# Kernel optimization log

Hardware: AMD Instinct MI355X
Metric: run time of the kernel (lower is better)

Reference implementation:

```python
import jax, jax.numpy as jnp
import numpy as np

H = 1024
NH = 16
DH = H // NH
EPS = 1e-12


def _heads(x):
    # [B,T,H] -> [B,NH,T,DH]
    B, T, _ = x.shape
    return x.reshape(B, T, NH, DH).transpose(0, 2, 1, 3)


def _layernorm(x, g, b):
    mu = jnp.mean(x, axis=-1, keepdims=True)
    var = jnp.mean(jnp.square(x - mu), axis=-1, keepdims=True)
    return (x - mu) * jax.lax.rsqrt(var + EPS) * g + b


def setup_inputs() -> dict:
    key = jax.random.key(0)
    ks = jax.random.split(key, 24)
    B, Tw, Te = 4, 1024, 128
    s = 0.02
    inp = {
        "word_hidden_states": jax.random.normal(ks[0], (B, Tw, H), jnp.float32),
        "entity_hidden_states": jax.random.normal(ks[1], (B, Te, H), jnp.float32),
        "attention_mask": jnp.zeros((B, 1, 1, Tw + Te), jnp.float32),
        "query_pos": jax.random.normal(ks[2], (B, Te, H), jnp.float32),
    }
    names = ["Wq", "Wk", "Wv", "Weq", "Wek", "Wev", "Wo", "Weo"]
    for i, n in enumerate(names):
        inp[n] = jax.random.normal(ks[3 + i], (H, H), jnp.float32) * s
        inp["b" + n[1:]] = jnp.zeros((H,), jnp.float32)
    inp["ln_g"] = jnp.ones((H,), jnp.float32)
    inp["ln_b"] = jnp.zeros((H,), jnp.float32)
    inp["eln_g"] = jnp.ones((H,), jnp.float32)
    inp["eln_b"] = jnp.zeros((H,), jnp.float32)
    return inp


def reference(word_hidden_states, entity_hidden_states, attention_mask, query_pos,
              Wq, bq, Wk, bk, Wv, bv, Weq, beq, Wek, bek, Wev, bev,
              Wo, bo, Weo, beo, ln_g, ln_b, eln_g, eln_b):
    Tw = word_hidden_states.shape[1]
    pos_ent = (entity_hidden_states + query_pos) * 0.5

    # per-stream projections (entity stream has its own e2w projections)
    qw = _heads(word_hidden_states @ Wq + bq)      # [B,NH,Tw,DH]
    qe = _heads(pos_ent @ Weq + beq)               # [B,NH,Te,DH]
    kw = _heads(word_hidden_states @ Wk + bk)
    ke = _heads(pos_ent @ Wek + bek)
    vw = _heads(word_hidden_states @ Wv + bv)
    ve = _heads(entity_hidden_states @ Wev + bev)  # value uses raw entity states

    q = jnp.concatenate([qw, qe], axis=2)          # [B,NH,T,DH]
    k = jnp.concatenate([kw, ke], axis=2)
    v = jnp.concatenate([vw, ve], axis=2)

    scores = jnp.einsum("bhqd,bhkd->bhqk", q, k) / np.sqrt(DH).astype(np.float32)
    scores = scores + attention_mask
    probs = jax.nn.softmax(scores, axis=-1)
    ctx = jnp.einsum("bhqk,bhkd->bhqd", probs, v)  # [B,NH,T,DH]
    B, _, T, _ = ctx.shape
    ctx = ctx.transpose(0, 2, 1, 3).reshape(B, T, H)

    word_self = ctx[:, :Tw, :]
    ent_self = ctx[:, Tw:, :]

    word_out = _layernorm(word_self @ Wo + bo + word_hidden_states, ln_g, ln_b)
    ent_out = _layernorm(ent_self @ Weo + beo + entity_hidden_states, eln_g, eln_b)
    return (word_out, ent_out)
```

## Files before the change

### kernel.cpp

```cpp
#include <hip/hip_runtime.h>
#include <math.h>

#define H_DIM 1024
#define NHEAD 16
#define DHEAD 64
#define T_W 1024
#define T_E 128
#define T_T 1152
#define BATCH 4

typedef __attribute__((ext_vector_type(8))) short s8b;
typedef __attribute__((ext_vector_type(4))) short s4b;
typedef __attribute__((ext_vector_type(4))) float f32x4;

#define LOG2E 1.44269504088896f

__device__ __forceinline__ unsigned short f2bf(float f) {
    unsigned int u = __float_as_uint(f);
    u = (u + 0x7fffu + ((u >> 16) & 1u)) >> 16;
    return (unsigned short)u;
}

__device__ __forceinline__ unsigned int pk_bf16(float a, float b) {
#if __has_builtin(__builtin_amdgcn_cvt_pk_bf16_f32)
    typedef __bf16 bf2 __attribute__((ext_vector_type(2)));
    bf2 r = __builtin_amdgcn_cvt_pk_bf16_f32(a, b);
    return __builtin_bit_cast(unsigned int, r);
#else
    return (unsigned int)f2bf(a) | ((unsigned int)f2bf(b) << 16);
#endif
}

__device__ __forceinline__ float exp2f_fast(float x) {
#if __has_builtin(__builtin_amdgcn_exp2f)
    return __builtin_amdgcn_exp2f(x);
#else
    return exp2f(x);
#endif
}

__device__ __forceinline__ void gld_lds16(const void* g, void* l) {
    __builtin_amdgcn_global_load_lds(
        (const __attribute__((address_space(1))) unsigned int*)g,
        (__attribute__((address_space(3))) unsigned int*)l, 16, 0, 0);
}

struct WPtrs { const float* w[8]; };
__global__ __launch_bounds__(256) void k_prep2(
    const float* __restrict__ word, const float* __restrict__ ent,
    const float* __restrict__ qp, const float* __restrict__ mask,
    unsigned short* __restrict__ word_bf, unsigned short* __restrict__ pe_bf,
    unsigned short* __restrict__ ent_bf, float* __restrict__ mask2,
    WPtrs ws, unsigned short* __restrict__ Wt)
{
    const int bid = blockIdx.x;
    if (bid < 4096) {
        int i = bid * 256 + threadIdx.x;
        float4 v = ((const float4*)word)[i];
        *(uint2*)(word_bf + (size_t)i * 4) =
            make_uint2(pk_bf16(v.x, v.y), pk_bf16(v.z, v.w));
    } else if (bid < 4608) {
        int i = (bid - 4096) * 256 + threadIdx.x;
        float4 a = ((const float4*)ent)[i];
        float4 b = ((const float4*)qp)[i];
        *(uint2*)(ent_bf + (size_t)i * 4) =
            make_uint2(pk_bf16(a.x, a.y), pk_bf16(a.z, a.w));
        *(uint2*)(pe_bf + (size_t)i * 4) =
            make_uint2(pk_bf16((a.x + b.x) * 0.5f, (a.y + b.y) * 0.5f),
                       pk_bf16((a.z + b.z) * 0.5f, (a.w + b.w) * 0.5f));
    } else if (bid < 4626) {
        int i = (bid - 4608) * 256 + threadIdx.x;
        if (i < BATCH * T_T) mask2[i] = mask[i] * LOG2E;
    } else {
        __shared__ float tile[32][33];
        const int id = bid - 4626;
        const int z = id >> 10, rem = id & 1023;
        const int kb = (rem >> 5) * 32, nb = (rem & 31) * 32;
        const float* src = ws.w[z];
        unsigned short* dst = Wt + (size_t)z * H_DIM * H_DIM;
        const int tx = threadIdx.x & 31, ty = threadIdx.x >> 5;
        #pragma unroll
        for (int i = 0; i < 4; i++)
            tile[ty * 4 + i][tx] = src[(size_t)(kb + ty * 4 + i) * H_DIM + nb + tx];
        __syncthreads();
        #pragma unroll
        for (int i = 0; i < 4; i++)
            dst[(size_t)(nb + ty * 4 + i) * H_DIM + kb + tx] =
                f2bf(tile[tx][ty * 4 + i]);
    }
}

struct B6 { const float* b[6]; };
struct O3p { void* o[3]; };


__global__ __launch_bounds__(256) void k_proj(
    const unsigned short* __restrict__ word_bf,
    const unsigned short* __restrict__ pe_bf,
    const unsigned short* __restrict__ ent_bf,
    const unsigned short* __restrict__ Wtbase, B6 biases, O3p outs)
{
    const int z = blockIdx.z;
    const bool isw = blockIdx.y < 64;
    const int Tseq = isw ? T_W : T_E;
    const int toff = isw ? 0 : T_W;
    const int m0 = (isw ? blockIdx.y : (blockIdx.y - 64)) * 64;
    const unsigned short* A = isw ? word_bf : (z == 2 ? ent_bf : pe_bf);
    const int wi = (isw ? 0 : 3) + z;
    const unsigned short* B = Wtbase + (size_t)wi * H_DIM * H_DIM;
    const float* bias = biases.b[wi];
    void* outp = outs.o[z];

    __shared__ unsigned short sm[12288];
    const int t = threadIdx.x;
    const int w = t >> 6, lane = t & 63;
    const int col = lane & 15, quad = lane >> 4;
    const int n0 = blockIdx.x * 128;
    const int wm = w & 1, wn = w >> 1;

    f32x4 acc[2][4] = {};

    const int rs = t >> 3;
    const int gch = (t & 7) ^ (rs & 7);
    const unsigned short* gA = A + (size_t)(m0 + rs) * H_DIM + gch * 8;
    const unsigned short* gB = B + (size_t)(n0 + rs) * H_DIM + gch * 8;

    for (int k0 = 0; k0 < H_DIM; k0 += 64) {
        gld_lds16(gA + k0, &sm[t * 8]);
        gld_lds16(gA + (size_t)32 * H_DIM + k0, &sm[2048 + t * 8]);
        gld_lds16(gB + k0, &sm[4096 + t * 8]);
        gld_lds16(gB + (size_t)32 * H_DIM + k0, &sm[6144 + t * 8]);
        gld_lds16(gB + (size_t)64 * H_DIM + k0, &sm[8192 + t * 8]);
        gld_lds16(gB + (size_t)96 * H_DIM + k0, &sm[10240 + t * 8]);
        __syncthreads();
        #pragma unroll
        for (int kk = 0; kk < 2; kk++) {
            s8b af[2], bfr[4];
            #pragma unroll
            for (int mt = 0; mt < 2; mt++) {
                const int r = wm * 32 + mt * 16 + col;
                af[mt] = *(const s8b*)&sm[r * 64 + (((kk * 4 + quad) ^ (r & 7)) * 8)];
            }
            #pragma unroll
            for (int nt = 0; nt < 4; nt++) {
                const int r = wn * 64 + nt * 16 + col;
                bfr[nt] = *(const s8b*)&sm[4096 + r * 64 +
                                           (((kk * 4 + quad) ^ (r & 7)) * 8)];
            }
            __builtin_amdgcn_s_setprio(1);
            #pragma unroll
            for (int mt = 0; mt < 2; mt++)
                #pragma unroll
                for (int nt = 0; nt < 4; nt++)
                    acc[mt][nt] = __builtin_amdgcn_mfma_f32_16x16x32_bf16(
                        af[mt], bfr[nt], acc[mt][nt], 0, 0, 0);
            __builtin_amdgcn_s_setprio(0);
        }
        __syncthreads();
    }

    #pragma unroll
    for (int mt = 0; mt < 2; mt++) {
        const int mg = m0 + wm * 32 + mt * 16 + quad * 4;
        const int b = mg / Tseq, tt = toff + (mg % Tseq);
        #pragma unroll
        for (int nt = 0; nt < 4; nt++) {
            const int ng = n0 + wn * 64 + nt * 16 + col;
            f32x4 c = acc[mt][nt];
            const float bn = bias[ng];
            if (z < 2) {
                unsigned short* out = (unsigned short*)outp;
                #pragma unroll
                for (int r = 0; r < 4; r++)
                    out[((size_t)b * T_T + tt + r) * H_DIM + ng] = f2bf(c[r] + bn);
            } else {
                unsigned short* out = (unsigned short*)outp;
                *(uint2*)(out + ((size_t)b * H_DIM + ng) * T_T + tt) =
                    make_uint2(pk_bf16(c[0] + bn, c[1] + bn),
                               pk_bf16(c[2] + bn, c[3] + bn));
            }
        }
    }
}

__global__ __launch_bounds__(256) void k_gemm_out(
    const unsigned short* __restrict__ ctx,
    const unsigned short* __restrict__ Wt_o, const unsigned short* __restrict__ Wt_eo,
    const float* __restrict__ bo, const float* __restrict__ beo,
    const float* __restrict__ word, const float* __restrict__ ent,
    float* __restrict__ out_word, float* __restrict__ out_ent)
{
    const int blk = blockIdx.x;
    const bool is_word = blk < 512;
    const int lb = is_word ? blk : blk - 512;
    const int m0 = (lb >> 3) * 64, n0 = (lb & 7) * 128;
    const unsigned short* B = is_word ? Wt_o : Wt_eo;
    const float* bias = is_word ? bo : beo;
    const float* resid = is_word ? word : ent;
    float* out = is_word ? out_word : out_ent;
    const int Tseq = is_word ? T_W : T_E;
    const int toff = is_word ? 0 : T_W;

    __shared__ unsigned short sm[12288];
    const int t = threadIdx.x;
    const int w = t >> 6, lane = t & 63;
    const int col = lane & 15, quad = lane >> 4;
    const int wm = w & 1, wn = w >> 1;

    f32x4 acc[2][4] = {};

    const int rs = t >> 3;
    const int gch = (t & 7) ^ (rs & 7);
    const size_t arow = (size_t)(m0 / Tseq) * T_T + toff + (m0 % Tseq) + rs;
    const unsigned short* gA = ctx + arow * H_DIM + gch * 8;
    const unsigned short* gB = B + (size_t)(n0 + rs) * H_DIM + gch * 8;

    for (int k0 = 0; k0 < H_DIM; k0 += 64) {
        gld_lds16(gA + k0, &sm[t * 8]);
        gld_lds16(gA + (size_t)32 * H_DIM + k0, &sm[2048 + t * 8]);
        gld_lds16(gB + k0, &sm[4096 + t * 8]);
        gld_lds16(gB + (size_t)32 * H_DIM + k0, &sm[6144 + t * 8]);
        gld_lds16(gB + (size_t)64 * H_DIM + k0, &sm[8192 + t * 8]);
        gld_lds16(gB + (size_t)96 * H_DIM + k0, &sm[10240 + t * 8]);
        __syncthreads();
        #pragma unroll
        for (int kk = 0; kk < 2; kk++) {
            s8b af[2], bfr[4];
            #pragma unroll
            for (int mt = 0; mt < 2; mt++) {
                const int r = wm * 32 + mt * 16 + col;
                af[mt] = *(const s8b*)&sm[r * 64 + (((kk * 4 + quad) ^ (r & 7)) * 8)];
            }
            #pragma unroll
            for (int nt = 0; nt < 4; nt++) {
                const int r = wn * 64 + nt * 16 + col;
                bfr[nt] = *(const s8b*)&sm[4096 + r * 64 +
                                           (((kk * 4 + quad) ^ (r & 7)) * 8)];
            }
            __builtin_amdgcn_s_setprio(1);
            #pragma unroll
            for (int mt = 0; mt < 2; mt++)
                #pragma unroll
                for (int nt = 0; nt < 4; nt++)
                    acc[mt][nt] = __builtin_amdgcn_mfma_f32_16x16x32_bf16(
                        af[mt], bfr[nt], acc[mt][nt], 0, 0, 0);
            __builtin_amdgcn_s_setprio(0);
        }
        __syncthreads();
    }

    #pragma unroll
    for (int mt = 0; mt < 2; mt++) {
        const int mg = m0 + wm * 32 + mt * 16 + quad * 4;
        #pragma unroll
        for (int nt = 0; nt < 4; nt++) {
            const int ng = n0 + wn * 64 + nt * 16 + col;
            f32x4 c = acc[mt][nt];
            const float bn = bias[ng];
            #pragma unroll
            for (int r = 0; r < 4; r++) {
                const size_t idx = (size_t)(mg + r) * H_DIM + ng;
                out[idx] = c[r] + bn + resid[idx];
            }
        }
    }
}

__global__ __launch_bounds__(512) void k_attn(
    const unsigned short* __restrict__ q, const unsigned short* __restrict__ k,
    const unsigned short* __restrict__ vt, const float* __restrict__ mask2,
    unsigned short* __restrict__ ctx)
{
    const int tid = threadIdx.x;
    const int w = tid >> 6, lane = tid & 63;
    const int col = lane & 15, quad = lane >> 4;
    const int bid = blockIdx.x;
    const int bh = ((bid & 7) << 3) | ((bid >> 3) & 7);
    const int q0 = (bid >> 6) * 128 + w * 16;
    const int b = bh >> 4, h = bh & 15;

    __shared__ unsigned short sK[2][64 * 64];
    __shared__ unsigned short sV[2][64 * 64];
    __shared__ __align__(16) unsigned short sP[8][16 * 64];
    unsigned short* sp = &sP[w][0];

    const unsigned short* qp = q + ((size_t)b * T_T + q0) * H_DIM + h * DHEAD;
    const unsigned short* kp = k + (size_t)b * T_T * H_DIM + h * DHEAD;
    const unsigned short* vp = vt + ((size_t)b * H_DIM + h * DHEAD) * T_T;
    const float* mp = mask2 + (size_t)b * T_T;

    const s8b qf0 = *(const s8b*)(qp + (size_t)col * H_DIM + quad * 8);
    const s8b qf1 = *(const s8b*)(qp + (size_t)col * H_DIM + 32 + quad * 8);

    const int rA = tid >> 3;
    const int cA = (tid & 7) ^ (rA & 7);

    const float SC2 = 0.125f * LOG2E;

    f32x4 O[4] = {};
    float l_part = 0.f;

    #define PREFETCH(J0, BUF)                                                        \
        {                                                                            \
            gld_lds16(kp + (size_t)((J0) + rA) * H_DIM + cA * 8,                     \
                      &sK[BUF][0] + tid * 8);                                        \
            gld_lds16(vp + (size_t)rA * T_T + (J0) + cA * 8,                         \
                      &sV[BUF][0] + tid * 8);                                        \
        }

    PREFETCH(0, 0)
    for (int it = 0; it < 18; it++) {
        const int j0 = it * 64;
        __syncthreads();
        if (it < 17) PREFETCH(j0 + 64, (it + 1) & 1)
        const unsigned short* K0 = &sK[it & 1][0];
        const unsigned short* V0 = &sV[it & 1][0];

        float p[16];
        #pragma unroll
        for (int kt = 0; kt < 4; kt++) {
            const int rk = kt * 16 + col;
            const int csw = quad ^ (rk & 7);
            s8b k0f = *(const s8b*)(K0 + rk * 64 + csw * 8);
            s8b k1f = *(const s8b*)(K0 + rk * 64 + (csw ^ 4) * 8);
            f32x4 z = {0.f, 0.f, 0.f, 0.f};
            __builtin_amdgcn_s_setprio(1);
            z = __builtin_amdgcn_mfma_f32_16x16x32_bf16(k0f, qf0, z, 0, 0, 0);
            z = __builtin_amdgcn_mfma_f32_16x16x32_bf16(k1f, qf1, z, 0, 0, 0);
            __builtin_amdgcn_s_setprio(0);
            float4 mv = *(const float4*)(mp + j0 + kt * 16 + quad * 4);
            float mvv[4] = {mv.x, mv.y, mv.z, mv.w};
            #pragma unroll
            for (int r = 0; r < 4; r++) {
                float pe = exp2f_fast(fmaf(z[r], SC2, mvv[r]));
                p[kt * 4 + r] = pe;
                l_part += pe;
            }
        }

        #pragma unroll
        for (int kt = 0; kt < 4; kt++) {
            const int chunk = 2 * kt + (quad >> 1);
            *(uint2*)(sp + col * 64 + ((chunk ^ (col & 7)) * 8) + (quad & 1) * 4) =
                make_uint2(pk_bf16(p[4 * kt], p[4 * kt + 1]),
                           pk_bf16(p[4 * kt + 2], p[4 * kt + 3]));
        }
        const s8b p0 = *(const s8b*)(sp + col * 64 + ((quad ^ (col & 7)) * 8));
        const s8b p1 = *(const s8b*)(sp + col * 64 + (((4 + quad) ^ (col & 7)) * 8));

        __builtin_amdgcn_s_setprio(1);
        #pragma unroll
        for (int dt = 0; dt < 4; dt++) {
            const int rf = dt * 16 + col;
            const int csw = quad ^ (rf & 7);
            s8b v0 = *(const s8b*)(V0 + rf * 64 + csw * 8);
            s8b v1 = *(const s8b*)(V0 + rf * 64 + (csw ^ 4) * 8);
            O[dt] = __builtin_amdgcn_mfma_f32_16x16x32_bf16(v0, p0, O[dt], 0, 0, 0);
            O[dt] = __builtin_amdgcn_mfma_f32_16x16x32_bf16(v1, p1, O[dt], 0, 0, 0);
        }
        __builtin_amdgcn_s_setprio(0);
    }
    #undef PREFETCH

    float l_c = l_part;
    l_c += __shfl_xor(l_c, 16);
    l_c += __shfl_xor(l_c, 32);
    const float inv = 1.f / l_c;
    unsigned short* ob = ctx + ((size_t)b * T_T + q0 + col) * H_DIM + h * DHEAD;
    #pragma unroll
    for (int dt = 0; dt < 4; dt++) {
        *(uint2*)(ob + dt * 16 + quad * 4) =
            make_uint2(pk_bf16(O[dt][0] * inv, O[dt][1] * inv),
                       pk_bf16(O[dt][2] * inv, O[dt][3] * inv));
    }
}

__global__ __launch_bounds__(256) void k_layernorm(float* __restrict__ x,
                                                   const float* __restrict__ g0,
                                                   const float* __restrict__ b0,
                                                   const float* __restrict__ g1,
                                                   const float* __restrict__ b1)
{
    const int row = blockIdx.x;
    const float* g = row < 4096 ? g0 : g1;
    const float* bta = row < 4096 ? b0 : b1;
    float* p = x + (size_t)row * H_DIM;
    const int t = threadIdx.x;
    float vals[4];
    float s = 0.f, ss = 0.f;
    #pragma unroll
    for (int i = 0; i < 4; i++) {
        float v = p[t + 256 * i];
        vals[i] = v;
        s += v;
        ss += v * v;
    }
    #pragma unroll
    for (int o = 32; o > 0; o >>= 1) {
        s += __shfl_xor(s, o);
        ss += __shfl_xor(ss, o);
    }
    __shared__ float red[2][4];
    const int wid = t >> 6, lane = t & 63;
    if (lane == 0) { red[0][wid] = s; red[1][wid] = ss; }
    __syncthreads();
    s = red[0][0] + red[0][1] + red[0][2] + red[0][3];
    ss = red[1][0] + red[1][1] + red[1][2] + red[1][3];
    float mu = s * (1.0f / H_DIM);
    float var = ss * (1.0f / H_DIM) - mu * mu;
    float r = rsqrtf(var + 1e-12f);
    #pragma unroll
    for (int i = 0; i < 4; i++) {
        int idx = t + 256 * i;
        p[idx] = (vals[i] - mu) * r * g[idx] + bta[idx];
    }
}

extern "C" void kernel_launch(void* const* d_in, const int* in_sizes, int n_in,
                              void* d_out, int out_size, void* d_ws, size_t ws_size,
                              hipStream_t stream) {
    const float* word = (const float*)d_in[0];
    const float* ent  = (const float*)d_in[1];
    const float* mask = (const float*)d_in[2];
    const float* qpos = (const float*)d_in[3];
    const float* Wq  = (const float*)d_in[4];  const float* bq  = (const float*)d_in[5];
    const float* Wk  = (const float*)d_in[6];  const float* bk  = (const float*)d_in[7];
    const float* Wv  = (const float*)d_in[8];  const float* bv  = (const float*)d_in[9];
    const float* Weq = (const float*)d_in[10]; const float* beq = (const float*)d_in[11];
    const float* Wek = (const float*)d_in[12]; const float* bek = (const float*)d_in[13];
    const float* Wev = (const float*)d_in[14]; const float* bev = (const float*)d_in[15];
    const float* Wo  = (const float*)d_in[16]; const float* bo  = (const float*)d_in[17];
    const float* Weo = (const float*)d_in[18]; const float* beo = (const float*)d_in[19];
    const float* ln_g  = (const float*)d_in[20]; const float* ln_b  = (const float*)d_in[21];
    const float* eln_g = (const float*)d_in[22]; const float* eln_b = (const float*)d_in[23];

    char* ws = (char*)d_ws;
    unsigned short* word_bf = (unsigned short*)(ws);
    unsigned short* pe_bf   = (unsigned short*)(ws + 8388608);
    unsigned short* ent_bf  = (unsigned short*)(ws + 9437184);
    float*          mask2   = (float*)(ws + 10466304);
    unsigned short* Wt      = (unsigned short*)(ws + 10485760);
    unsigned short* qb      = (unsigned short*)(ws + 27262976);
    unsigned short* kb      = (unsigned short*)(ws + 36700160);
    unsigned short* vt      = (unsigned short*)(ws + 46137344);
    unsigned short* ctx     = (unsigned short*)(ws + 55574528);

    float* out_word = (float*)d_out;
    float* out_ent  = out_word + 4194304;

    const size_t WSZ = (size_t)H_DIM * H_DIM;
    unsigned short* Wt_o  = Wt + 6 * WSZ;
    unsigned short* Wt_eo = Wt + 7 * WSZ;

    WPtrs wp = {{Wq, Wk, Wv, Weq, Wek, Wev, Wo, Weo}};
    k_prep2<<<dim3(12818), 256, 0, stream>>>(word, ent, qpos, mask,
                                             word_bf, pe_bf, ent_bf, mask2, wp, Wt);

    B6 bb = {{bq, bk, bv, beq, bek, bev}};
    O3p ow = {{qb, kb, vt}};
    k_proj<<<dim3(8, 72, 3), 256, 0, stream>>>(word_bf, pe_bf, ent_bf, Wt, bb, ow);

    k_attn<<<dim3(NHEAD * BATCH * 9), 512, 0, stream>>>(qb, kb, vt, mask2, ctx);

    k_gemm_out<<<dim3(576), 256, 0, stream>>>(ctx, Wt_o, Wt_eo, bo, beo,
                                              word, ent, out_word, out_ent);

    k_layernorm<<<dim3(4608), 256, 0, stream>>>(out_word, ln_g, ln_b, eln_g, eln_b);
}
```

Before: 261.4 us.

## Double-buffer LDS tiles in projection and output GEMMs to overlap loads with MFMA

Both GEMM kernels now use two LDS buffers and prefetch the next K-tile via global-to-LDS loads while computing on the current one. The goal is to hide global load latency behind the MFMA work and drop one barrier per iteration. LDS per block doubles to 48 KB, which may cut occupancy. The single barrier at the end of each iteration may not guarantee the async loads have finished before the buffer is read.

Result: no change. 261.5 us (+0.0%).

```diff
diff --git a/kernel.cpp b/kernel.cpp
--- a/kernel.cpp
+++ b/kernel.cpp
@@ -94,6 +94,16 @@
 struct O3p { void* o[3]; };
 
 
+#define STAGE_GEMM(k0, base)                                                     \
+    {                                                                            \
+        gld_lds16(gA + (k0), &sm[(base) + t * 8]);                               \
+        gld_lds16(gA + (size_t)32 * H_DIM + (k0), &sm[(base) + 2048 + t * 8]);   \
+        gld_lds16(gB + (k0), &sm[(base) + 4096 + t * 8]);                        \
+        gld_lds16(gB + (size_t)32 * H_DIM + (k0), &sm[(base) + 6144 + t * 8]);   \
+        gld_lds16(gB + (size_t)64 * H_DIM + (k0), &sm[(base) + 8192 + t * 8]);   \
+        gld_lds16(gB + (size_t)96 * H_DIM + (k0), &sm[(base) + 10240 + t * 8]);  \
+    }
+
 __global__ __launch_bounds__(256) void k_proj(
     const unsigned short* __restrict__ word_bf,
     const unsigned short* __restrict__ pe_bf,
@@ -111,7 +121,7 @@
     const float* bias = biases.b[wi];
     void* outp = outs.o[z];
 
-    __shared__ unsigned short sm[12288];
+    __shared__ unsigned short sm[24576];
     const int t = threadIdx.x;
     const int w = t >> 6, lane = t & 63;
     const int col = lane & 15, quad = lane >> 4;
@@ -125,26 +135,24 @@
     const unsigned short* gA = A + (size_t)(m0 + rs) * H_DIM + gch * 8;
     const unsigned short* gB = B + (size_t)(n0 + rs) * H_DIM + gch * 8;
 
+    STAGE_GEMM(0, 0)
+    __syncthreads();
+    int base = 0;
     for (int k0 = 0; k0 < H_DIM; k0 += 64) {
-        gld_lds16(gA + k0, &sm[t * 8]);
-        gld_lds16(gA + (size_t)32 * H_DIM + k0, &sm[2048 + t * 8]);
-        gld_lds16(gB + k0, &sm[4096 + t * 8]);
-        gld_lds16(gB + (size_t)32 * H_DIM + k0, &sm[6144 + t * 8]);
-        gld_lds16(gB + (size_t)64 * H_DIM + k0, &sm[8192 + t * 8]);
-        gld_lds16(gB + (size_t)96 * H_DIM + k0, &sm[10240 + t * 8]);
-        __syncthreads();
+        if (k0 + 64 < H_DIM) STAGE_GEMM(k0 + 64, base ^ 12288)
         #pragma unroll
         for (int kk = 0; kk < 2; kk++) {
             s8b af[2], bfr[4];
             #pragma unroll
             for (int mt = 0; mt < 2; mt++) {
                 const int r = wm * 32 + mt * 16 + col;
-                af[mt] = *(const s8b*)&sm[r * 64 + (((kk * 4 + quad) ^ (r & 7)) * 8)];
+                af[mt] = *(const s8b*)&sm[base + r * 64 +
+                                          (((kk * 4 + quad) ^ (r & 7)) * 8)];
             }
             #pragma unroll
             for (int nt = 0; nt < 4; nt++) {
                 const int r = wn * 64 + nt * 16 + col;
-                bfr[nt] = *(const s8b*)&sm[4096 + r * 64 +
+                bfr[nt] = *(const s8b*)&sm[base + 4096 + r * 64 +
                                            (((kk * 4 + quad) ^ (r & 7)) * 8)];
             }
             __builtin_amdgcn_s_setprio(1);
@@ -157,6 +165,7 @@
             __builtin_amdgcn_s_setprio(0);
         }
         __syncthreads();
+        base ^= 12288;
     }
 
     #pragma unroll
@@ -201,7 +210,7 @@
     const int Tseq = is_word ? T_W : T_E;
     const int toff = is_word ? 0 : T_W;
 
-    __shared__ unsigned short sm[12288];
+    __shared__ unsigned short sm[24576];
     const int t = threadIdx.x;
     const int w = t >> 6, lane = t & 63;
     const int col = lane & 15, quad = lane >> 4;
@@ -215,26 +224,24 @@
     const unsigned short* gA = ctx + arow * H_DIM + gch * 8;
     const unsigned short* gB = B + (size_t)(n0 + rs) * H_DIM + gch * 8;
 
+    STAGE_GEMM(0, 0)
+    __syncthreads();
+    int base = 0;
     for (int k0 = 0; k0 < H_DIM; k0 += 64) {
-        gld_lds16(gA + k0, &sm[t * 8]);
-        gld_lds16(gA + (size_t)32 * H_DIM + k0, &sm[2048 + t * 8]);
-        gld_lds16(gB + k0, &sm[4096 + t * 8]);
-        gld_lds16(gB + (size_t)32 * H_DIM + k0, &sm[6144 + t * 8]);
-        gld_lds16(gB + (size_t)64 * H_DIM + k0, &sm[8192 + t * 8]);
-        gld_lds16(gB + (size_t)96 * H_DIM + k0, &sm[10240 + t * 8]);
-        __syncthreads();
+        if (k0 + 64 < H_DIM) STAGE_GEMM(k0 + 64, base ^ 12288)
         #pragma unroll
         for (int kk = 0; kk < 2; kk++) {
             s8b af[2], bfr[4];
             #pragma unroll
             for (int mt = 0; mt < 2; mt++) {
                 const int r = wm * 32 + mt * 16 + col;
-                af[mt] = *(const s8b*)&sm[r * 64 + (((kk * 4 + quad) ^ (r & 7)) * 8)];
+                af[mt] = *(const s8b*)&sm[base + r * 64 +
+                                          (((kk * 4 + quad) ^ (r & 7)) * 8)];
             }
             #pragma unroll
             for (int nt = 0; nt < 4; nt++) {
                 const int r = wn * 64 + nt * 16 + col;
-                bfr[nt] = *(const s8b*)&sm[4096 + r * 64 +
+                bfr[nt] = *(const s8b*)&sm[base + 4096 + r * 64 +
                                            (((kk * 4 + quad) ^ (r & 7)) * 8)];
             }
             __builtin_amdgcn_s_setprio(1);
@@ -247,6 +254,7 @@
             __builtin_amdgcn_s_setprio(0);
         }
         __syncthreads();
+        base ^= 12288;
     }
 
     #pragma unroll
```
